# Optimization experiments

Measured on AMD Instinct MI355X. Metric: run time of the kernel, lower is better.

The kernel has to match this reference:

```python
import jax, jax.numpy as jnp
import numpy as np

B, T = 32, 1024
AC, SE, H, NH = 20, 16, 64, 4
HD = H // NH  # 16


def setup_inputs() -> dict:
    key = jax.random.key(0)
    ks = jax.random.split(key, 8)
    g = 0.1  # xavier gain used in _init_weights (rough scale)
    return {
        'acoustic': jax.random.normal(ks[0], (B, T, AC), jnp.float32),
        'semantic': jax.random.normal(ks[1], (B, T, SE), jnp.float32),
        'Wq': jax.random.normal(ks[2], (H, SE), jnp.float32) * g,
        'bq': jnp.zeros((H,), jnp.float32),
        'Wkv': jax.random.normal(ks[3], (2 * H, AC), jnp.float32) * g,
        'bkv': jnp.zeros((2 * H,), jnp.float32),
        'in_w': jax.random.normal(ks[4], (3 * H, H), jnp.float32) * g,
        'in_b': jnp.zeros((3 * H,), jnp.float32),
        'out_w': jax.random.normal(ks[5], (H, H), jnp.float32) * g,
        'out_b': jnp.zeros((H,), jnp.float32),
        'proj_w': jax.random.normal(ks[6], (AC, H), jnp.float32) * g,
        'proj_b': jnp.zeros((AC,), jnp.float32),
        'residual_logit': jnp.float32(-2.0),
        'ln_gamma': jnp.ones((AC,), jnp.float32),
        'ln_beta': jnp.zeros((AC,), jnp.float32),
    }


def _std(x, axis, keepdims=True):
    # torch.std default: unbiased (ddof=1)
    return jnp.std(x, axis=axis, ddof=1, keepdims=keepdims)


def reference(acoustic, semantic, Wq, bq, Wkv, bkv, in_w, in_b, out_w, out_b,
              proj_w, proj_b, residual_logit, ln_gamma, ln_beta):
    # projections to hidden space
    q = semantic @ Wq.T + bq                       # [B,T,H]
    kv = acoustic @ Wkv.T + bkv                    # [B,T,2H]
    k, v = kv[..., :H], kv[..., H:]
    # nn.MultiheadAttention in-projection
    qi = q @ in_w[:H].T + in_b[:H]
    ki = k @ in_w[H:2 * H].T + in_b[H:2 * H]
    vi = v @ in_w[2 * H:].T + in_b[2 * H:]
    # split heads -> [B,T,NH,HD]
    qh = qi.reshape(B, T, NH, HD)
    kh = ki.reshape(B, T, NH, HD)
    vh = vi.reshape(B, T, NH, HD)
    scores = jnp.einsum('bqhd,bkhd->bhqk', qh, kh) / jnp.sqrt(jnp.float32(HD))
    attn = jax.nn.softmax(scores, axis=-1)         # [B,NH,T,T]
    ctx = jnp.einsum('bhqk,bkhd->bqhd', attn, vh).reshape(B, T, H)
    attended = ctx @ out_w.T + out_b               # MHA out_proj
    enhanced_raw = attended @ proj_w.T + proj_b    # [B,T,AC]
    enhanced = acoustic + jax.nn.sigmoid(residual_logit) * enhanced_raw

    # statistics over batch+time (no_grad in torch -> stop_gradient)
    orig_mean = jax.lax.stop_gradient(jnp.mean(acoustic, axis=(0, 1), keepdims=True))
    orig_std = jax.lax.stop_gradient(_std(acoustic, (0, 1)) + 1e-8)
    a_n = (acoustic - orig_mean) / orig_std
    e_n = (enhanced - orig_mean) / orig_std
    std_ratio = _std(e_n, (0, 1)) / (_std(a_n, (0, 1)) + 1e-8)
    std_corr = jnp.where(std_ratio < 0.4, 0.4 / std_ratio, jnp.ones_like(std_ratio))
    enhanced_final = (e_n * std_corr) * orig_std + orig_mean

    # LayerNorm over last dim (biased variance, eps=1e-5)
    mu = jnp.mean(enhanced_final, axis=-1, keepdims=True)
    var = jnp.mean(jnp.square(enhanced_final - mu), axis=-1, keepdims=True)
    return (enhanced_final - mu) * jax.lax.rsqrt(var + 1e-5) * ln_gamma + ln_beta
```

## Files before the change

### kernel.cpp

```cpp
#include <hip/hip_runtime.h>
#include <hip/hip_bf16.h>
#include <math.h>

#define B 32
#define T 1024
#define AC 20
#define SE 16
#define H 64
#define NH 4
#define HD 16
#define NROW (B*T)
#define BH (B*NH)
#define NCHUNK (T/32)
#define NSLOT 128

typedef unsigned short u16;
typedef short short8 __attribute__((ext_vector_type(8)));
typedef float f32x16 __attribute__((ext_vector_type(16)));
typedef unsigned int uintx4 __attribute__((ext_vector_type(4)));

#define F_QB   (BH*T*16/2)
#define OFF_KB   0
#define OFF_VT   (OFF_KB + F_QB)
#define OFF_ET   (OFF_VT + F_QB)
#define OFF_WF   (OFF_ET + AC*NROW)
#define OFF_ACC  (OFF_WF + 5120)
#define OFF_ST   (OFF_ACC + NSLOT*80)

#define WF_WQ 0
#define WF_BQ 1024
#define WF_WK 1088
#define WF_BK 2368
#define WF_WV 2432
#define WF_BV 3712
#define WF_WO 3776
#define WF_BO 5056
#define WF_TOTAL 5076

__device__ __forceinline__ u16 bf16b(float a) {
    __hip_bfloat16 t = __float2bfloat16(a);
    u16 u; __builtin_memcpy(&u, &t, 2); return u;
}
__device__ __forceinline__ unsigned packbf(float a, float b) {
    return (unsigned)bf16b(a) | ((unsigned)bf16b(b) << 16);
}

__global__ __launch_bounds__(256) void k_fuse(
    const float* __restrict__ Wq, const float* __restrict__ bq,
    const float* __restrict__ Wkv, const float* __restrict__ bkv,
    const float* __restrict__ in_w, const float* __restrict__ in_b,
    const float* __restrict__ out_w, const float* __restrict__ out_b,
    const float* __restrict__ proj_w, const float* __restrict__ proj_b,
    float* __restrict__ wf, float* __restrict__ accum) {
    int idx = blockIdx.x * 256 + threadIdx.x;
    if (idx < NSLOT*40) {
        accum[idx] = 0.f;
        accum[idx + NSLOT*40] = 0.f;
    }
    if (idx >= WF_TOTAL) return;
    if (idx < WF_BQ) {
        int i = idx >> 4, j = idx & 15;
        float s = 0.f;
        for (int m = 0; m < H; ++m) s += in_w[i*H + m] * Wq[m*SE + j];
        wf[idx] = 0.25f * s;
    } else if (idx < WF_WK) {
        int i = idx - WF_BQ;
        float s = in_b[i];
        for (int m = 0; m < H; ++m) s += in_w[i*H + m] * bq[m];
        wf[idx] = 0.25f * s;
    } else if (idx < WF_BK) {
        int r = idx - WF_WK; int i = r / AC, j = r % AC;
        float s = 0.f;
        for (int m = 0; m < H; ++m) s += in_w[(H+i)*H + m] * Wkv[m*AC + j];
        wf[idx] = s;
    } else if (idx < WF_WV) {
        int i = idx - WF_BK;
        float s = in_b[H + i];
        for (int m = 0; m < H; ++m) s += in_w[(H+i)*H + m] * bkv[m];
        wf[idx] = s;
    } else if (idx < WF_BV) {
        int r = idx - WF_WV; int i = r / AC, j = r % AC;
        float s = 0.f;
        for (int m = 0; m < H; ++m) s += in_w[(2*H+i)*H + m] * Wkv[(H+m)*AC + j];
        wf[idx] = s;
    } else if (idx < WF_WO) {
        int i = idx - WF_BV;
        float s = in_b[2*H + i];
        for (int m = 0; m < H; ++m) s += in_w[(2*H+i)*H + m] * bkv[H + m];
        wf[idx] = s;
    } else if (idx < WF_BO) {
        int r = idx - WF_WO; int c = r >> 6, d = r & 63;
        float s = 0.f;
        for (int m = 0; m < H; ++m) s += proj_w[c*H + m] * out_w[m*H + d];
        wf[idx] = s;
    } else {
        int c = idx - WF_BO;
        float s = proj_b[c];
        for (int m = 0; m < H; ++m) s += proj_w[c*H + m] * out_b[m];
        wf[idx] = s;
    }
}

__global__ __launch_bounds__(128) void k_qkv(
    const float* __restrict__ acst, const float* __restrict__ wf,
    u16* __restrict__ Kb, u16* __restrict__ Vtb) {
    __shared__ __align__(16) unsigned vls32[16*33];
    const int tid = threadIdx.x;
    const int sec = tid >> 4, r = tid & 15;
    const int row = blockIdx.x * 16 + r;
    const int b = row >> 10, t = row & 1023;
    const int type = sec >> 2, h = sec & 3;
    float o[16];
    {
        float a[AC];
        const float4* ap = (const float4*)(acst + (size_t)row * AC);
        #pragma unroll
        for (int i = 0; i < 5; ++i) {
            float4 v = ap[i];
            a[4*i] = v.x; a[4*i+1] = v.y; a[4*i+2] = v.z; a[4*i+3] = v.w;
        }
        const float* wb = wf + (type == 0 ? WF_WK : WF_WV) + h*16*AC;
        const float* bb = wf + (type == 0 ? WF_BK : WF_BV) + h*16;
        #pragma unroll
        for (int ii = 0; ii < 16; ++ii) {
            float acc = bb[ii];
            #pragma unroll
            for (int j = 0; j < 5; ++j) {
                float4 w4 = *(const float4*)(wb + ii*AC + 4*j);
                acc += a[4*j]*w4.x + a[4*j+1]*w4.y + a[4*j+2]*w4.z + a[4*j+3]*w4.w;
            }
            o[ii] = acc;
        }
    }
    if (type == 0) {
        unsigned* dst = (unsigned*)(Kb + (((size_t)(b*NH + h))*T + t)*16);
        #pragma unroll
        for (int i = 0; i < 8; ++i) dst[i] = packbf(o[2*i], o[2*i+1]);
    } else {
        u16* v16 = (u16*)vls32;
        #pragma unroll
        for (int d = 0; d < HD; ++d) v16[d*66 + h*16 + r] = bf16b(o[d]);
    }
    __syncthreads();
    if (type == 1) {
        const int l = tid - 64, h2 = l >> 4, li = l & 15;
        const int bb_ = blockIdx.x >> 6, g = blockIdx.x & 63;
        unsigned tmp[8];
        #pragma unroll
        for (int k = 0; k < 8; ++k) tmp[k] = vls32[li*33 + h2*8 + k];
        unsigned* dst = (unsigned*)(Vtb + ((size_t)((bb_*NH + h2)*64 + g))*256) + li*8;
        *(uintx4*)dst       = (uintx4){tmp[0], tmp[1], tmp[2], tmp[3]};
        *(uintx4*)(dst + 4) = (uintx4){tmp[4], tmp[5], tmp[6], tmp[7]};
    }
}

#define CSTR 66
__global__ __launch_bounds__(256, 4) void k_attn(
    const float* __restrict__ sem,
    const u16* __restrict__ Kb, const u16* __restrict__ Vtb,
    const float* __restrict__ acst, const float* __restrict__ wf,
    const float* __restrict__ rlogit,
    float* __restrict__ enhT, float* __restrict__ accum) {
    __shared__ __align__(16) float ctxs[32*CSTR];
    __shared__ __align__(16) float wsm[AC*H + AC];
    __shared__ __align__(16) float wqs[16*H + H];
    const int tid  = threadIdx.x;
    const int lane = tid & 63;
    const int wv   = tid >> 6;
    for (int i = tid; i < AC*H + AC; i += 256) wsm[i] = wf[WF_WO + i];
    for (int i = tid; i < 16*H + H; i += 256) wqs[i] = wf[WF_WQ + i];
    const int blk  = blockIdx.x;
    const int b    = blk & 31;
    const int qblk = blk >> 5;
    const int l31 = lane & 31, hi2 = lane >> 5, l15 = lane & 15;
    const int bh = b*NH + wv;
    const int q0 = qblk*32;
    __syncthreads();

    short8 qf;
    {
        float s[SE];
        const float4* sp = (const float4*)(sem + ((size_t)b*T + q0 + l31) * SE);
        #pragma unroll
        for (int i = 0; i < 4; ++i) {
            float4 v = sp[i];
            s[4*i] = v.x; s[4*i+1] = v.y; s[4*i+2] = v.z; s[4*i+3] = v.w;
        }
        #pragma unroll
        for (int jj = 0; jj < 8; ++jj) {
            const int ii = wv*16 + hi2*8 + jj;
            float acc = wqs[1024 + ii];
            #pragma unroll
            for (int j = 0; j < 4; ++j) {
                float4 w4 = *(const float4*)(wqs + ii*SE + 4*j);
                acc += s[4*j]*w4.x + s[4*j+1]*w4.y + s[4*j+2]*w4.z + s[4*j+3]*w4.w;
            }
            qf[jj] = (short)bf16b(acc);
        }
    }

    const u16* kp = Kb + ((size_t)bh*T + l31)*16 + 8*hi2;
    const u16* vp = Vtb + (size_t)bh*16384 + l15*16 + 8*hi2;

    f32x16 acc = {0.f,0.f,0.f,0.f,0.f,0.f,0.f,0.f,0.f,0.f,0.f,0.f,0.f,0.f,0.f,0.f};
    const f32x16 z16 = {0.f,0.f,0.f,0.f,0.f,0.f,0.f,0.f,0.f,0.f,0.f,0.f,0.f,0.f,0.f,0.f};
    float ls = 0.f;

    short8 kf = *(const short8*)kp;
    short8 va = *(const short8*)vp;
    short8 vb = *(const short8*)(vp + 256);
    #pragma unroll 4
    for (int ch = 0; ch < NCHUNK; ++ch) {
        const int nx = (ch < NCHUNK-1) ? ch + 1 : ch;
        short8 kf_n = *(const short8*)(kp + (size_t)nx*512);
        short8 va_n = *(const short8*)(vp + (size_t)nx*512);
        short8 vb_n = *(const short8*)(vp + (size_t)nx*512 + 256);

        f32x16 sc = __builtin_amdgcn_mfma_f32_32x32x16_bf16(kf, qf, z16, 0, 0, 0);
        float p[16];
        #pragma unroll
        for (int r = 0; r < 16; ++r) p[r] = __expf(sc[r]);
        #pragma unroll
        for (int r = 0; r < 16; ++r) ls += p[r];

        unsigned u0 = packbf(p[0],  p[1]);
        unsigned u1 = packbf(p[2],  p[3]);
        unsigned u2 = packbf(p[4],  p[5]);
        unsigned u3 = packbf(p[6],  p[7]);
        unsigned u4 = packbf(p[8],  p[9]);
        unsigned u5 = packbf(p[10], p[11]);
        unsigned u6 = packbf(p[12], p[13]);
        unsigned u7 = packbf(p[14], p[15]);
        asm("v_permlane32_swap_b32 %0, %1" : "+v"(u2), "+v"(u0));
        asm("v_permlane32_swap_b32 %0, %1" : "+v"(u3), "+v"(u1));
        asm("v_permlane32_swap_b32 %0, %1" : "+v"(u6), "+v"(u4));
        asm("v_permlane32_swap_b32 %0, %1" : "+v"(u7), "+v"(u5));
        uintx4 t1 = {u0, u1, u2, u3};
        uintx4 t2 = {u4, u5, u6, u7};
        short8 pf1 = __builtin_bit_cast(short8, t1);
        short8 pf2 = __builtin_bit_cast(short8, t2);

        acc = __builtin_amdgcn_mfma_f32_32x32x16_bf16(va, pf1, acc, 0, 0, 0);
        acc = __builtin_amdgcn_mfma_f32_32x32x16_bf16(vb, pf2, acc, 0, 0, 0);

        kf = kf_n; va = va_n; vb = vb_n;
    }

    ls += __shfl_xor(ls, 32);
    const float inv = 1.f / ls;
    #pragma unroll
    for (int r = 0; r < 8; ++r) {
        const int d = (r & 3) + 8*(r >> 2) + 4*hi2;
        ctxs[l31*CSTR + wv*16 + d] = acc[r] * inv;
    }
    __syncthreads();

    const int rq = tid & 31, g = tid >> 5;
    const int row = b*T + q0 + rq;
    const float sg = 1.f / (1.f + __expf(-rlogit[0]));
    float* slot = accum + (size_t)(blk & (NSLOT-1)) * 80;
    const int nj = (g < 4) ? 3 : 2;
    for (int j = 0; j < nj; ++j) {
        const int ch = g + 8*j;
        float s = wsm[AC*H + ch];
        #pragma unroll
        for (int kc = 0; kc < 4; ++kc) {
            float c0 = ctxs[rq*CSTR + kc*16 +  0], c1 = ctxs[rq*CSTR + kc*16 +  1];
            float c2 = ctxs[rq*CSTR + kc*16 +  2], c3 = ctxs[rq*CSTR + kc*16 +  3];
            float c4 = ctxs[rq*CSTR + kc*16 +  4], c5 = ctxs[rq*CSTR + kc*16 +  5];
            float c6 = ctxs[rq*CSTR + kc*16 +  6], c7 = ctxs[rq*CSTR + kc*16 +  7];
            float c8 = ctxs[rq*CSTR + kc*16 +  8], c9 = ctxs[rq*CSTR + kc*16 +  9];
            float cA = ctxs[rq*CSTR + kc*16 + 10], cB = ctxs[rq*CSTR + kc*16 + 11];
            float cC = ctxs[rq*CSTR + kc*16 + 12], cD = ctxs[rq*CSTR + kc*16 + 13];
            float cE = ctxs[rq*CSTR + kc*16 + 14], cF = ctxs[rq*CSTR + kc*16 + 15];
            const float* w = wsm + ch*H + kc*16;
            s += c0*w[0] + c1*w[1] + c2*w[2] + c3*w[3]
               + c4*w[4] + c5*w[5] + c6*w[6] + c7*w[7]
               + c8*w[8] + c9*w[9] + cA*w[10] + cB*w[11]
               + cC*w[12] + cD*w[13] + cE*w[14] + cF*w[15];
        }
        const float a = acst[(size_t)row*AC + ch];
        const float e = a + sg * s;
        enhT[(size_t)ch * NROW + row] = e;
        float sa = a, qa = a*a, se = e, qe = e*e;
        #pragma unroll
        for (int m = 1; m <= 16; m <<= 1) {
            sa += __shfl_xor(sa, m); qa += __shfl_xor(qa, m);
            se += __shfl_xor(se, m); qe += __shfl_xor(qe, m);
        }
        if (rq == 0) {
            atomicAdd(&slot[ch*4+0], sa);
            atomicAdd(&slot[ch*4+1], qa);
            atomicAdd(&slot[ch*4+2], se);
            atomicAdd(&slot[ch*4+3], qe);
        }
    }
}

__global__ __launch_bounds__(640) void k_stats2(
    const float* __restrict__ accum, float* __restrict__ stats) {
    __shared__ float red[80*8];
    __shared__ float acs[80];
    const int tx = threadIdx.x;
    const int c = tx >> 3, p = tx & 7;
    float s0 = 0.f, s1 = 0.f, s2 = 0.f, s3 = 0.f;
    #pragma unroll
    for (int i = 0; i < 4; ++i) {
        int sl = p + (4*i)*8;
        s0 += accum[(size_t)sl*80 + c];
        s1 += accum[(size_t)(sl+8)*80 + c];
        s2 += accum[(size_t)(sl+16)*80 + c];
        s3 += accum[(size_t)(sl+24)*80 + c];
    }
    red[c*8 + p] = (s0 + s1) + (s2 + s3);
    __syncthreads();
    if (tx < 80) {
        float t = 0.f;
        #pragma unroll
        for (int i = 0; i < 8; ++i) t += red[tx*8 + i];
        acs[tx] = t;
    }
    __syncthreads();
    if (tx < AC) {
        const float Nf = (float)NROW;
        float sa = acs[tx*4+0], qa = acs[tx*4+1];
        float se = acs[tx*4+2], qe = acs[tx*4+3];
        float mu  = sa / Nf;
        float va  = (qa - sa*sa/Nf) / (Nf - 1.f);
        float sda = sqrtf(fmaxf(va, 0.f));
        float osd = sda + 1e-8f;
        float ve  = (qe - se*se/Nf) / (Nf - 1.f);
        float sde = sqrtf(fmaxf(ve, 0.f));
        float ratio = (sde / osd) / (sda / osd + 1e-8f);
        float corr  = (ratio < 0.4f) ? (0.4f / ratio) : 1.f;
        stats[tx*2]   = mu;
        stats[tx*2+1] = corr;
    }
}

__global__ __launch_bounds__(128) void k_final(
    const float* __restrict__ enhT, const float* __restrict__ stats,
    const float* __restrict__ gamma, const float* __restrict__ beta,
    float* __restrict__ out) {
    __shared__ float acs[40];
    const int tx = threadIdx.x;
    if (tx < 40) acs[tx] = stats[tx];
    __syncthreads();
    int row = blockIdx.x * 128 + tx;
    float ef[AC];
    #pragma unroll
    for (int c = 0; c < AC; ++c) {
        float mu = acs[c*2], corr = acs[c*2+1];
        float e = enhT[(size_t)c * NROW + row];
        ef[c] = (e - mu) * corr + mu;
    }
    float m = 0.f;
    #pragma unroll
    for (int c = 0; c < AC; ++c) m += ef[c];
    m *= (1.f / AC);
    float v = 0.f;
    #pragma unroll
    for (int c = 0; c < AC; ++c) { float d = ef[c] - m; v += d*d; }
    v *= (1.f / AC);
    float inv = rsqrtf(v + 1e-5f);
    float o[AC];
    #pragma unroll
    for (int c = 0; c < AC; ++c) o[c] = (ef[c] - m) * inv * gamma[c] + beta[c];
    float4* op = (float4*)(out + (size_t)row * AC);
    #pragma unroll
    for (int i = 0; i < 5; ++i)
        op[i] = make_float4(o[4*i], o[4*i+1], o[4*i+2], o[4*i+3]);
}

extern "C" void kernel_launch(void* const* d_in, const int* in_sizes, int n_in,
                              void* d_out, int out_size, void* d_ws, size_t ws_size,
                              hipStream_t stream) {
    (void)in_sizes; (void)n_in; (void)out_size; (void)ws_size;
    const float* acoustic = (const float*)d_in[0];
    const float* semantic = (const float*)d_in[1];
    const float* Wq     = (const float*)d_in[2];
    const float* bq     = (const float*)d_in[3];
    const float* Wkv    = (const float*)d_in[4];
    const float* bkv    = (const float*)d_in[5];
    const float* in_w   = (const float*)d_in[6];
    const float* in_b   = (const float*)d_in[7];
    const float* out_w  = (const float*)d_in[8];
    const float* out_b  = (const float*)d_in[9];
    const float* proj_w = (const float*)d_in[10];
    const float* proj_b = (const float*)d_in[11];
    const float* rlogit = (const float*)d_in[12];
    const float* gamma  = (const float*)d_in[13];
    const float* beta   = (const float*)d_in[14];
    float* ws = (float*)d_ws;
    u16* Kb  = (u16*)(ws + OFF_KB);
    u16* Vtb = (u16*)(ws + OFF_VT);
    float* enhT  = ws + OFF_ET;
    float* wf    = ws + OFF_WF;
    float* accum = ws + OFF_ACC;
    float* stats = ws + OFF_ST;
    float* out = (float*)d_out;

    k_fuse<<<(WF_TOTAL + 255)/256, 256, 0, stream>>>(Wq, bq, Wkv, bkv, in_w, in_b,
                                                     out_w, out_b, proj_w, proj_b, wf, accum);
    k_qkv<<<NROW/16, 128, 0, stream>>>(acoustic, wf, Kb, Vtb);
    k_attn<<<1024, 256, 0, stream>>>(semantic, Kb, Vtb, acoustic, wf, rlogit, enhT, accum);
    k_stats2<<<1, 640, 0, stream>>>(accum, stats);
    k_final<<<NROW/128, 128, 0, stream>>>(enhT, stats, gamma, beta, out);
}
```

Measured before the change: 149.3 us.

## Fold softmax row-sum into PV MFMA via ones column in V tile

The V-transposed buffer is widened to 32 rows per tile, and the extra rows are filled with bf16 ones, so the PV MFMA also produces the softmax denominator. This removes the 16 scalar adds per chunk and the cross-lane shuffle reduction. The main loop is also restructured into a two-chunk software pipeline with deeper prefetch. The cost is twice the V memory traffic, half of it wasted MFMA columns, and higher register pressure.

```diff
diff --git a/kernel.cpp b/kernel.cpp
--- a/kernel.cpp
+++ b/kernel.cpp
@@ -19,10 +19,11 @@
 typedef float f32x16 __attribute__((ext_vector_type(16)));
 typedef unsigned int uintx4 __attribute__((ext_vector_type(4)));
 
-#define F_QB   (BH*T*16/2)
+#define F_KB   (BH*T*16/2)
+#define F_VT   (BH*32768/2)
 #define OFF_KB   0
-#define OFF_VT   (OFF_KB + F_QB)
-#define OFF_ET   (OFF_VT + F_QB)
+#define OFF_VT   (OFF_KB + F_KB)
+#define OFF_ET   (OFF_VT + F_VT)
 #define OFF_WF   (OFF_ET + AC*NROW)
 #define OFF_ACC  (OFF_WF + 5120)
 #define OFF_ST   (OFF_ACC + NSLOT*80)
@@ -145,12 +146,19 @@
     if (type == 1) {
         const int l = tid - 64, h2 = l >> 4, li = l & 15;
         const int bb_ = blockIdx.x >> 6, g = blockIdx.x & 63;
+        const size_t tile = (size_t)((bb_*NH + h2)*64 + g);
         unsigned tmp[8];
         #pragma unroll
         for (int k = 0; k < 8; ++k) tmp[k] = vls32[li*33 + h2*8 + k];
-        unsigned* dst = (unsigned*)(Vtb + ((size_t)((bb_*NH + h2)*64 + g))*256) + li*8;
+        unsigned* dst = (unsigned*)(Vtb + tile*512) + li*8;
         *(uintx4*)dst       = (uintx4){tmp[0], tmp[1], tmp[2], tmp[3]};
         *(uintx4*)(dst + 4) = (uintx4){tmp[4], tmp[5], tmp[6], tmp[7]};
+        if (li == 0) {
+            unsigned* od = (unsigned*)(Vtb + tile*512 + 256);
+            const unsigned one2 = 0x3F803F80u;
+            *(uintx4*)od       = (uintx4){one2, one2, one2, one2};
+            *(uintx4*)(od + 4) = (uintx4){one2, one2, one2, one2};
+        }
     }
 }
 
@@ -172,7 +180,7 @@
     const int blk  = blockIdx.x;
     const int b    = blk & 31;
     const int qblk = blk >> 5;
-    const int l31 = lane & 31, hi2 = lane >> 5, l15 = lane & 15;
+    const int l31 = lane & 31, hi2 = lane >> 5;
     const int bh = b*NH + wv;
     const int q0 = qblk*32;
     __syncthreads();
@@ -189,40 +197,27 @@
         #pragma unroll
         for (int jj = 0; jj < 8; ++jj) {
             const int ii = wv*16 + hi2*8 + jj;
-            float acc = wqs[1024 + ii];
+            float acc0 = wqs[1024 + ii];
             #pragma unroll
             for (int j = 0; j < 4; ++j) {
                 float4 w4 = *(const float4*)(wqs + ii*SE + 4*j);
-                acc += s[4*j]*w4.x + s[4*j+1]*w4.y + s[4*j+2]*w4.z + s[4*j+3]*w4.w;
+                acc0 += s[4*j]*w4.x + s[4*j+1]*w4.y + s[4*j+2]*w4.z + s[4*j+3]*w4.w;
             }
-            qf[jj] = (short)bf16b(acc);
+            qf[jj] = (short)bf16b(acc0);
         }
     }
 
     const u16* kp = Kb + ((size_t)bh*T + l31)*16 + 8*hi2;
-    const u16* vp = Vtb + (size_t)bh*16384 + l15*16 + 8*hi2;
+    const u16* vp = Vtb + (size_t)bh*32768 + l31*16 + 8*hi2;
 
     f32x16 acc = {0.f,0.f,0.f,0.f,0.f,0.f,0.f,0.f,0.f,0.f,0.f,0.f,0.f,0.f,0.f,0.f};
     const f32x16 z16 = {0.f,0.f,0.f,0.f,0.f,0.f,0.f,0.f,0.f,0.f,0.f,0.f,0.f,0.f,0.f,0.f};
-    float ls = 0.f;
-
-    short8 kf = *(const short8*)kp;
-    short8 va = *(const short8*)vp;
-    short8 vb = *(const short8*)(vp + 256);
-    #pragma unroll 4
-    for (int ch = 0; ch < NCHUNK; ++ch) {
-        const int nx = (ch < NCHUNK-1) ? ch + 1 : ch;
-        short8 kf_n = *(const short8*)(kp + (size_t)nx*512);
-        short8 va_n = *(const short8*)(vp + (size_t)nx*512);
-        short8 vb_n = *(const short8*)(vp + (size_t)nx*512 + 256);
-
+
+    auto chunk = [&](short8 kf, short8 va, short8 vb) {
         f32x16 sc = __builtin_amdgcn_mfma_f32_32x32x16_bf16(kf, qf, z16, 0, 0, 0);
         float p[16];
         #pragma unroll
         for (int r = 0; r < 16; ++r) p[r] = __expf(sc[r]);
-        #pragma unroll
-        for (int r = 0; r < 16; ++r) ls += p[r];
-
         unsigned u0 = packbf(p[0],  p[1]);
         unsigned u1 = packbf(p[2],  p[3]);
         unsigned u2 = packbf(p[4],  p[5]);
@@ -239,14 +234,32 @@
         uintx4 t2 = {u4, u5, u6, u7};
         short8 pf1 = __builtin_bit_cast(short8, t1);
         short8 pf2 = __builtin_bit_cast(short8, t2);
-
         acc = __builtin_amdgcn_mfma_f32_32x32x16_bf16(va, pf1, acc, 0, 0, 0);
         acc = __builtin_amdgcn_mfma_f32_32x32x16_bf16(vb, pf2, acc, 0, 0, 0);
-
-        kf = kf_n; va = va_n; vb = vb_n;
-    }
-
-    ls += __shfl_xor(ls, 32);
+    };
+
+    short8 kfA = *(const short8*)kp;
+    short8 vaA = *(const short8*)vp;
+    short8 vbA = *(const short8*)(vp + 512);
+    short8 kfB = *(const short8*)(kp + 512);
+    short8 vaB = *(const short8*)(vp + 1024);
+    short8 vbB = *(const short8*)(vp + 1536);
+    for (int ch = 0; ch < NCHUNK; ch += 2) {
+        const int n0 = (ch + 2 < NCHUNK) ? ch + 2 : ch;
+        short8 kfN0 = *(const short8*)(kp + (size_t)n0*512);
+        short8 vaN0 = *(const short8*)(vp + (size_t)n0*1024);
+        short8 vbN0 = *(const short8*)(vp + (size_t)n0*1024 + 512);
+        chunk(kfA, vaA, vbA);
+        const int n1 = (ch + 3 < NCHUNK) ? ch + 3 : ch + 1;
+        short8 kfN1 = *(const short8*)(kp + (size_t)n1*512);
+        short8 vaN1 = *(const short8*)(vp + (size_t)n1*1024);
+        short8 vbN1 = *(const short8*)(vp + (size_t)n1*1024 + 512);
+        chunk(kfB, vaB, vbB);
+        kfA = kfN0; vaA = vaN0; vbA = vbN0;
+        kfB = kfN1; vaB = vaN1; vbB = vbN1;
+    }
+
+    const float ls = __shfl(acc[8], l31);
     const float inv = 1.f / ls;
     #pragma unroll
     for (int r = 0; r < 8; ++r) {
```

After: 145.6 us. 1.03x faster.
